# Kernel tuning notes

Measured on AMD Instinct MI355X. Metric: run time of the kernel, lower is better.

The kernel has to match this reference:

```python
import jax, jax.numpy as jnp
import numpy as np

EPS = 1e-6      # delta in ixaxaar/pytorch-dnc util.py and Memory.reset
CLIP = 20.0     # DNC default controller-output clip
M, Wc, R, H, IN, OUT = 10, 20, 1, 256, 27, 128
NN_IN = IN + R * Wc                 # 47 controller input size
IFACE = R * Wc + 3 * Wc + 5 * R + 3  # 88 interface vector size


def _cosine_weights(mem, keys, strengths):
    # mem (B,M,Wc), keys (B,K,Wc), strengths (B,K) -> softmax over cells of scaled cosine sim
    mem_n = mem / (jnp.linalg.norm(mem, axis=2, keepdims=True) + EPS)
    key_n = keys / (jnp.linalg.norm(keys, axis=2, keepdims=True) + EPS)
    d = jnp.einsum('bkw,bmw->bkm', key_n, mem_n)
    return jax.nn.softmax(d * strengths[:, :, None], axis=2)


def _dnc_classifier(x, W_ih, W_hh, b_ih, b_hh, W_xi, b_xi, W_fc, b_fc):
    B, T, _ = x.shape
    # ixaxaar's dnc.py builds inputs[t] = cat(x_t, last_read) ONCE with the initial
    # (zero) last_read, so read vectors never feed the next-step input.
    pad = jnp.zeros((B, R * Wc), x.dtype)
    eye_mask = 1.0 - jnp.eye(M, dtype=x.dtype)

    def step(state, x_t):
        h, c, mem, link, prec, rw, ww, usage = state
        # ---- LSTM controller (1 hidden layer, torch gate order i,f,g,o) ----
        inp = jnp.concatenate([x_t, pad], axis=1)                 # (B,47)
        gates = inp @ W_ih.T + b_ih + h @ W_hh.T + b_hh           # (B,4H)
        i, f, g, o = jnp.split(gates, 4, axis=1)
        c = jax.nn.sigmoid(f) * c + jax.nn.sigmoid(i) * jnp.tanh(g)
        h = jax.nn.sigmoid(o) * jnp.tanh(c)
        out = jnp.clip(h, -CLIP, CLIP)
        # ---- interface vector ----
        xi = out @ W_xi.T + b_xi                                  # (B,88)
        p = R * Wc
        rk = jnp.tanh(xi[:, :p]).reshape(B, R, Wc)                # read keys
        rs = jax.nn.softplus(xi[:, p:p + R]); p += R              # read strengths
        wk = jnp.tanh(xi[:, p:p + Wc]).reshape(B, 1, Wc); p += Wc # write key
        ws = jax.nn.softplus(xi[:, p:p + 1]); p += 1              # write strength
        ev = jax.nn.sigmoid(xi[:, p:p + Wc]); p += Wc             # erase vector
        wv = jnp.tanh(xi[:, p:p + Wc]); p += Wc                   # write vector
        fg = jax.nn.sigmoid(xi[:, p:p + R]); p += R               # free gates
        ag = jax.nn.sigmoid(xi[:, p:p + 1]); p += 1               # allocation gate
        wg = jax.nn.sigmoid(xi[:, p:p + 1]); p += 1               # write gate
        rm = jax.nn.softmax(xi[:, p:p + 3 * R].reshape(B, R, 3), axis=-1)  # read modes (b,f,c)
        # ---- usage (uses PREVIOUS write/read weights) ----
        usage = usage + (1 - usage) * ww
        usage = usage * jnp.prod(1 - fg[:, :, None] * rw, axis=1)
        # ---- write weighting: content + allocation (sort-based free list) ----
        cw = _cosine_weights(mem, wk, ws)[:, 0]                   # (B,M)
        u2 = EPS + (1 - EPS) * usage
        phi = jnp.argsort(u2, axis=1)
        su = jnp.take_along_axis(u2, phi, axis=1)
        prod_excl = jnp.cumprod(jnp.concatenate([jnp.ones((B, 1), u2.dtype), su], axis=1), axis=1)[:, :-1]
        alloc = jnp.take_along_axis((1 - su) * prod_excl, jnp.argsort(phi, axis=1), axis=1)
        ww = wg * (ag * alloc + (1 - ag) * cw)                    # (B,M)
        # ---- erase + write memory ----
        mem = mem * (1 - ww[:, :, None] * ev[:, None, :]) + ww[:, :, None] * wv[:, None, :]
        # ---- temporal link matrix + precedence ----
        link = (1 - ww[:, :, None] - ww[:, None, :]) * link + ww[:, :, None] * prec[:, None, :]
        link = link * eye_mask
        prec = (1 - jnp.sum(ww, axis=1, keepdims=True)) * prec + ww
        # ---- read weighting (content + forward/backward temporal) ----
        cwr = _cosine_weights(mem, rk, rs)                        # (B,R,M)
        fw = jnp.einsum('brm,bnm->brn', rw, link)                 # forward  = L @ w
        bw = jnp.einsum('brm,bmn->brn', rw, link)                 # backward = L^T @ w
        rw = rm[:, :, 0:1] * bw + rm[:, :, 1:2] * fw + rm[:, :, 2:3] * cwr
        return (h, c, mem, link, prec, rw, ww, usage), None

    z = jnp.zeros
    state0 = (z((B, H), x.dtype), z((B, H), x.dtype),
              jnp.full((B, M, Wc), EPS, x.dtype), z((B, M, M), x.dtype),
              z((B, M), x.dtype), jnp.full((B, R, M), EPS, x.dtype),
              jnp.full((B, M), EPS, x.dtype), z((B, M), x.dtype))
    (h, *_), _ = jax.lax.scan(step, state0, jnp.swapaxes(x, 0, 1))
    # classifier head: fc1 on final controller hidden state
    return h @ W_fc.T + b_fc


def setup_inputs() -> dict:
    key = jax.random.key(0)
    ks = jax.random.split(key, 10)
    B, T = 128, 512
    kb = 1.0 / np.sqrt(H)
    u = lambda kk, shape: jax.random.uniform(kk, shape, jnp.float32, -kb, kb)
    return {
        'x': jax.random.normal(ks[0], (B, T, IN), jnp.float32),
        'input_lengths': jax.random.randint(ks[1], (B,), 1, T + 1).astype(jnp.int32),
        'W_ih': u(ks[2], (4 * H, NN_IN)),
        'W_hh': u(ks[3], (4 * H, H)),
        'b_ih': u(ks[4], (4 * H,)),
        'b_hh': u(ks[5], (4 * H,)),
        'W_xi': u(ks[6], (IFACE, H)),
        'b_xi': u(ks[7], (IFACE,)),
        'W_fc': u(ks[8], (OUT, H)),
        'b_fc': u(ks[9], (OUT,)),
    }


def reference(x, input_lengths, W_ih, W_hh, b_ih, b_hh, W_xi, b_xi, W_fc, b_fc):
    # input_lengths is unpacked and discarded by DNCClassifier.forward
    return _dnc_classifier(x, W_ih, W_hh, b_ih, b_hh, W_xi, b_xi, W_fc, b_fc)
```

## Files before the change

### kernel.cpp

```cpp
#include <hip/hip_runtime.h>
#include <hip/hip_fp16.h>


typedef _Float16 h2t __attribute__((ext_vector_type(2)));
typedef unsigned int u32x4 __attribute__((ext_vector_type(4)));

#if defined(__has_builtin)
#  if __has_builtin(__builtin_amdgcn_fdot2)
#    define HAVE_FDOT2 1
#  endif
#endif

__device__ __forceinline__ h2t bc2(unsigned int v) {
  union { unsigned int u; h2t h; } x; x.u = v; return x.h;
}
__device__ __forceinline__ unsigned int pk(float a, float b) {
  union { h2t h; unsigned int u; } x;
  x.h[0] = (_Float16)a; x.h[1] = (_Float16)b;
  return x.u;
}
__device__ __forceinline__ float fdot2f(h2t a, h2t b, float c) {
#ifdef HAVE_FDOT2
  return __builtin_amdgcn_fdot2(a, b, c, false);
#else
  return c + (float)a[0] * (float)b[0] + (float)a[1] * (float)b[1];
#endif
}
__device__ __forceinline__ float dot4(u32x4 w, u32x4 h, float a) {
  a = fdot2f(bc2(w[0]), bc2(h[0]), a);
  a = fdot2f(bc2(w[1]), bc2(h[1]), a);
  a = fdot2f(bc2(w[2]), bc2(h[2]), a);
  a = fdot2f(bc2(w[3]), bc2(h[3]), a);
  return a;
}
__device__ __forceinline__ float sigmf_(float x) {
  return 1.f / (1.f + __expf(-x));
}
__device__ __forceinline__ float tanhf_(float x) {
  float xc = fminf(15.f, fmaxf(-15.f, x));
  float e = __expf(2.f * xc);
  return (e - 1.f) / (e + 1.f);
}

#define WS_P_OFF 0ull
#define WS_W_OFF 134217728ull
#define WS_NEED  134742016ull

__global__ void prep_w(const float* __restrict__ W_hh,
                       unsigned char* __restrict__ ws) {
  int j = blockIdx.x * 256 + threadIdx.x;
  int e = j & 3, v = (j >> 2) & 511, f = j >> 11;
  int jq = f >> 2, g = f & 3;
  int w = v >> 6, l = v & 63;
  int half = w >> 2;
  int u = ((w & 3) << 6) + l;
  int k2 = 64 * half + 4 * jq + e;
  int r = g * 256 + u;
  ((unsigned int*)(ws + WS_W_OFF))[j] =
      pk(W_hh[r * 256 + 2 * k2], W_hh[r * 256 + 2 * k2 + 1]);
}

__global__ __launch_bounds__(256) void prep_p(const float* __restrict__ x,
                                              const float* __restrict__ W_ih,
                                              const float* __restrict__ b_ih,
                                              const float* __restrict__ b_hh,
                                              unsigned char* __restrict__ ws) {
  __shared__ unsigned int sX[64][14];
  const int u = threadIdx.x;
  const int t = blockIdx.x >> 1;
  const int b0 = (blockIdx.x & 1) << 6;
  unsigned int wih[4][14];
  float bias[4];
#pragma unroll
  for (int g = 0; g < 4; ++g) {
    const float* row = W_ih + (size_t)(g * 256 + u) * 47;
    bias[g] = b_ih[g * 256 + u] + b_hh[g * 256 + u];
#pragma unroll
    for (int j = 0; j < 14; ++j) {
      float a = row[2 * j];
      float b = (2 * j + 1 < 27) ? row[2 * j + 1] : 0.f;
      wih[g][j] = pk(a, b);
    }
  }
#pragma unroll 1
  for (int j = u; j < 896; j += 256) {
    int row = j / 14, c2 = j - 14 * row;
    const float* xr = x + ((size_t)(b0 + row) * 512 + t) * 27;
    float a = xr[2 * c2];
    float bb = (2 * c2 + 1 < 27) ? xr[2 * c2 + 1] : 0.f;
    sX[row][c2] = pk(a, bb);
  }
  __syncthreads();
  uint2* Pout = (uint2*)(ws + WS_P_OFF);
#pragma unroll 2
  for (int p = 0; p < 64; ++p) {
    float a0 = bias[0], a1 = bias[1], a2 = bias[2], a3 = bias[3];
#pragma unroll
    for (int j = 0; j < 14; ++j) {
      h2t xx = bc2(sX[p][j]);
      a0 = fdot2f(bc2(wih[0][j]), xx, a0);
      a1 = fdot2f(bc2(wih[1][j]), xx, a1);
      a2 = fdot2f(bc2(wih[2][j]), xx, a2);
      a3 = fdot2f(bc2(wih[3][j]), xx, a3);
    }
    uint2 o; o.x = pk(a0, a1); o.y = pk(a2, a3);
    Pout[((size_t)t * 128 + (b0 + p)) * 256 + u] = o;
  }
}

#define JHB(jq, W0, W1, W2, W3)        \
  {                                    \
    u32x4 hq = rd[jq];                 \
    acc0 = dot4(W0, hq, acc0);         \
    acc1 = dot4(W1, hq, acc1);         \
    acc2 = dot4(W2, hq, acc2);         \
    acc3 = dot4(W3, hq, acc3);         \
  }

__global__ __launch_bounds__(512) void scan_k(
    const unsigned char* __restrict__ ws, const float* __restrict__ W_fc,
    const float* __restrict__ b_fc, float* __restrict__ out) {
  __shared__ u32x4 sW[18 * 512];
  __shared__ u32x4 sHq[2][32];
  __shared__ float4 sRed[256];
  __shared__ float sHF[256];
  const int v = threadIdx.x, b = blockIdx.x;
  const int w = v >> 6, l = v & 63;
  const int half = w >> 2;
  const int u = ((w & 3) << 6) + l;
  const bool upd = (half == 0);
  const u32x4* Wq = (const u32x4*)(ws + WS_W_OFF);

  u32x4 wr[18];
#pragma unroll
  for (int f = 0; f < 18; ++f) wr[f] = Wq[f * 512 + v];
#pragma unroll
  for (int f = 0; f < 18; ++f) sW[f * 512 + v] = Wq[(18 + f) * 512 + v];
  if (v < 64) {
    u32x4 z = {0u, 0u, 0u, 0u};
    ((u32x4*)sHq)[v] = z;
  }

  const uint2* Pbuf = (const uint2*)(ws + WS_P_OFF);
  uint2 pP = make_uint2(0u, 0u);
  if (upd) pP = Pbuf[(size_t)b * 256 + u];
  float c = 0.f, hval = 0.f;
  __syncthreads();

#pragma unroll 1
  for (int t = 0; t < 512; ++t) {
    u32x4 sa0 = Wq[36 * 512 + v], sa1 = Wq[37 * 512 + v];
    u32x4 sa2 = Wq[38 * 512 + v], sa3 = Wq[39 * 512 + v];
    u32x4 sb0 = Wq[40 * 512 + v], sb1 = Wq[41 * 512 + v];
    u32x4 sb2 = Wq[42 * 512 + v], sb3 = Wq[43 * 512 + v];

    const u32x4* rd = &sHq[t & 1][half << 4];
    float acc0 = 0.f, acc1 = 0.f, acc2 = 0.f, acc3 = 0.f;
    JHB(0, wr[0], wr[1], wr[2], wr[3]);
    JHB(1, wr[4], wr[5], wr[6], wr[7]);
    JHB(2, wr[8], wr[9], wr[10], wr[11]);
    JHB(3, wr[12], wr[13], wr[14], wr[15]);
    JHB(4, wr[16], wr[17], sW[0 * 512 + v], sW[1 * 512 + v]);
    JHB(5, sW[2 * 512 + v], sW[3 * 512 + v], sW[4 * 512 + v], sW[5 * 512 + v]);
    JHB(6, sW[6 * 512 + v], sW[7 * 512 + v], sW[8 * 512 + v], sW[9 * 512 + v]);
    JHB(7, sW[10 * 512 + v], sW[11 * 512 + v], sW[12 * 512 + v], sW[13 * 512 + v]);
    JHB(8, sW[14 * 512 + v], sW[15 * 512 + v], sW[16 * 512 + v], sW[17 * 512 + v]);
    JHB(9, sa0, sa1, sa2, sa3);
    sa0 = Wq[44 * 512 + v]; sa1 = Wq[45 * 512 + v];
    sa2 = Wq[46 * 512 + v]; sa3 = Wq[47 * 512 + v];
    JHB(10, sb0, sb1, sb2, sb3);
    sb0 = Wq[48 * 512 + v]; sb1 = Wq[49 * 512 + v];
    sb2 = Wq[50 * 512 + v]; sb3 = Wq[51 * 512 + v];
    JHB(11, sa0, sa1, sa2, sa3);
    sa0 = Wq[52 * 512 + v]; sa1 = Wq[53 * 512 + v];
    sa2 = Wq[54 * 512 + v]; sa3 = Wq[55 * 512 + v];
    JHB(12, sb0, sb1, sb2, sb3);
    sb0 = Wq[56 * 512 + v]; sb1 = Wq[57 * 512 + v];
    sb2 = Wq[58 * 512 + v]; sb3 = Wq[59 * 512 + v];
    JHB(13, sa0, sa1, sa2, sa3);
    sa0 = Wq[60 * 512 + v]; sa1 = Wq[61 * 512 + v];
    sa2 = Wq[62 * 512 + v]; sa3 = Wq[63 * 512 + v];
    JHB(14, sb0, sb1, sb2, sb3);
    JHB(15, sa0, sa1, sa2, sa3);

    if (!upd) sRed[u] = make_float4(acc0, acc1, acc2, acc3);
    __syncthreads();

    if (upd) {
      float4 o = sRed[u];
      h2t p01 = bc2(pP.x), p23 = bc2(pP.y);
      float gi = acc0 + o.x + (float)p01[0];
      float gf = acc1 + o.y + (float)p01[1];
      float gg = acc2 + o.z + (float)p23[0];
      float go = acc3 + o.w + (float)p23[1];
      c = sigmf_(gf) * c + sigmf_(gi) * tanhf_(gg);
      hval = sigmf_(go) * tanhf_(c);
      ((_Float16*)(&sHq[(t + 1) & 1][0]))[u] = (_Float16)hval;
      if (t == 511) sHF[u] = hval;
      int tn = (t < 511) ? t + 1 : 511;
      pP = Pbuf[((size_t)tn * 128 + b) * 256 + u];
    }
    __syncthreads();
  }

  if (v < 128) {
    const float4* wrow = (const float4*)(W_fc + (size_t)v * 256);
    float a = b_fc[v];
#pragma unroll 8
    for (int q = 0; q < 64; ++q) {
      float4 wv = wrow[q];
      float4 hh = ((const float4*)sHF)[q];
      a += wv.x * hh.x + wv.y * hh.y + wv.z * hh.z + wv.w * hh.w;
    }
    out[(size_t)b * 128 + v] = a;
  }
}

extern "C" void kernel_launch(void* const* d_in, const int* in_sizes, int n_in,
                              void* d_out, int out_size, void* d_ws,
                              size_t ws_size, hipStream_t stream) {
  const float* x    = (const float*)d_in[0];
  const float* W_ih = (const float*)d_in[2];
  const float* W_hh = (const float*)d_in[3];
  const float* b_ih = (const float*)d_in[4];
  const float* b_hh = (const float*)d_in[5];
  const float* W_fc = (const float*)d_in[8];
  const float* b_fc = (const float*)d_in[9];
  unsigned char* ws = (unsigned char*)d_ws;

  if (ws_size < WS_NEED) return;

  prep_w<<<512, 256, 0, stream>>>(W_hh, ws);
  prep_p<<<1024, 256, 0, stream>>>(x, W_ih, b_ih, b_hh, ws);
  scan_k<<<128, 512, 0, stream>>>(ws, W_fc, b_fc, (float*)d_out);
}
```

Measured before the change: 913.3 us.

## Process two batch elements per scan block to reuse loaded recurrent weights

Each scan block now handles two batch rows instead of one. Every weight fragment, whether held in registers, LDS or fetched from global memory, is dotted against both hidden states, and each half of the block finishes the gate update for one element. This halves the grid to 64 blocks and doubles the arithmetic per weight load. The cost is more accumulator registers, fewer weights kept in registers (16 instead of 18), and each block's serial per-step critical path roughly doubles in dot-product work.

After: 1.490 ms. 63.2% more time.

```diff
diff --git a/kernel.cpp b/kernel.cpp
--- a/kernel.cpp
+++ b/kernel.cpp
@@ -108,111 +108,115 @@
   }
 }
 
-#define JHB(jq, W0, W1, W2, W3)        \
-  {                                    \
-    u32x4 hq = rd[jq];                 \
-    acc0 = dot4(W0, hq, acc0);         \
-    acc1 = dot4(W1, hq, acc1);         \
-    acc2 = dot4(W2, hq, acc2);         \
-    acc3 = dot4(W3, hq, acc3);         \
+#define JH2(jq, W0, W1, W2, W3)          \
+  {                                      \
+    u32x4 hM = rdM[jq], hO = rdO[jq];    \
+    aM0 = dot4(W0, hM, aM0);             \
+    aO0 = dot4(W0, hO, aO0);             \
+    aM1 = dot4(W1, hM, aM1);             \
+    aO1 = dot4(W1, hO, aO1);             \
+    aM2 = dot4(W2, hM, aM2);             \
+    aO2 = dot4(W2, hO, aO2);             \
+    aM3 = dot4(W3, hM, aM3);             \
+    aO3 = dot4(W3, hO, aO3);             \
   }
 
 __global__ __launch_bounds__(512) void scan_k(
     const unsigned char* __restrict__ ws, const float* __restrict__ W_fc,
     const float* __restrict__ b_fc, float* __restrict__ out) {
   __shared__ u32x4 sW[18 * 512];
-  __shared__ u32x4 sHq[2][32];
-  __shared__ float4 sRed[256];
-  __shared__ float sHF[256];
-  const int v = threadIdx.x, b = blockIdx.x;
+  __shared__ u32x4 sH[2][2][32];
+  __shared__ float4 sRed[2][256];
+  __shared__ float sHF[2][256];
+  const int v = threadIdx.x, b0 = blockIdx.x * 2;
   const int w = v >> 6, l = v & 63;
   const int half = w >> 2;
   const int u = ((w & 3) << 6) + l;
-  const bool upd = (half == 0);
+  const int me = half, ot = half ^ 1;
   const u32x4* Wq = (const u32x4*)(ws + WS_W_OFF);
 
-  u32x4 wr[18];
-#pragma unroll
-  for (int f = 0; f < 18; ++f) wr[f] = Wq[f * 512 + v];
-#pragma unroll
-  for (int f = 0; f < 18; ++f) sW[f * 512 + v] = Wq[(18 + f) * 512 + v];
-  if (v < 64) {
-    u32x4 z = {0u, 0u, 0u, 0u};
-    ((u32x4*)sHq)[v] = z;
-  }
+  u32x4 wr[16];
+#pragma unroll
+  for (int f = 0; f < 16; ++f) wr[f] = Wq[f * 512 + v];
+#pragma unroll
+  for (int f = 0; f < 18; ++f) sW[f * 512 + v] = Wq[(16 + f) * 512 + v];
+  if (v < 128) ((u32x4*)sH)[v] = u32x4{0u, 0u, 0u, 0u};
 
   const uint2* Pbuf = (const uint2*)(ws + WS_P_OFF);
-  uint2 pP = make_uint2(0u, 0u);
-  if (upd) pP = Pbuf[(size_t)b * 256 + u];
+  uint2 pP = Pbuf[((size_t)0 * 128 + (b0 + me)) * 256 + u];
   float c = 0.f, hval = 0.f;
   __syncthreads();
 
 #pragma unroll 1
   for (int t = 0; t < 512; ++t) {
-    u32x4 sa0 = Wq[36 * 512 + v], sa1 = Wq[37 * 512 + v];
-    u32x4 sa2 = Wq[38 * 512 + v], sa3 = Wq[39 * 512 + v];
-    u32x4 sb0 = Wq[40 * 512 + v], sb1 = Wq[41 * 512 + v];
-    u32x4 sb2 = Wq[42 * 512 + v], sb3 = Wq[43 * 512 + v];
-
-    const u32x4* rd = &sHq[t & 1][half << 4];
-    float acc0 = 0.f, acc1 = 0.f, acc2 = 0.f, acc3 = 0.f;
-    JHB(0, wr[0], wr[1], wr[2], wr[3]);
-    JHB(1, wr[4], wr[5], wr[6], wr[7]);
-    JHB(2, wr[8], wr[9], wr[10], wr[11]);
-    JHB(3, wr[12], wr[13], wr[14], wr[15]);
-    JHB(4, wr[16], wr[17], sW[0 * 512 + v], sW[1 * 512 + v]);
-    JHB(5, sW[2 * 512 + v], sW[3 * 512 + v], sW[4 * 512 + v], sW[5 * 512 + v]);
-    JHB(6, sW[6 * 512 + v], sW[7 * 512 + v], sW[8 * 512 + v], sW[9 * 512 + v]);
-    JHB(7, sW[10 * 512 + v], sW[11 * 512 + v], sW[12 * 512 + v], sW[13 * 512 + v]);
-    JHB(8, sW[14 * 512 + v], sW[15 * 512 + v], sW[16 * 512 + v], sW[17 * 512 + v]);
-    JHB(9, sa0, sa1, sa2, sa3);
-    sa0 = Wq[44 * 512 + v]; sa1 = Wq[45 * 512 + v];
-    sa2 = Wq[46 * 512 + v]; sa3 = Wq[47 * 512 + v];
-    JHB(10, sb0, sb1, sb2, sb3);
-    sb0 = Wq[48 * 512 + v]; sb1 = Wq[49 * 512 + v];
-    sb2 = Wq[50 * 512 + v]; sb3 = Wq[51 * 512 + v];
-    JHB(11, sa0, sa1, sa2, sa3);
-    sa0 = Wq[52 * 512 + v]; sa1 = Wq[53 * 512 + v];
-    sa2 = Wq[54 * 512 + v]; sa3 = Wq[55 * 512 + v];
-    JHB(12, sb0, sb1, sb2, sb3);
-    sb0 = Wq[56 * 512 + v]; sb1 = Wq[57 * 512 + v];
-    sb2 = Wq[58 * 512 + v]; sb3 = Wq[59 * 512 + v];
-    JHB(13, sa0, sa1, sa2, sa3);
-    sa0 = Wq[60 * 512 + v]; sa1 = Wq[61 * 512 + v];
-    sa2 = Wq[62 * 512 + v]; sa3 = Wq[63 * 512 + v];
-    JHB(14, sb0, sb1, sb2, sb3);
-    JHB(15, sa0, sa1, sa2, sa3);
-
-    if (!upd) sRed[u] = make_float4(acc0, acc1, acc2, acc3);
+    u32x4 t0 = Wq[34 * 512 + v], t1 = Wq[35 * 512 + v];
+    u32x4 t2 = Wq[36 * 512 + v], t3 = Wq[37 * 512 + v];
+    u32x4 t4 = Wq[38 * 512 + v], t5 = Wq[39 * 512 + v];
+    u32x4 t6 = Wq[40 * 512 + v], t7 = Wq[41 * 512 + v];
+
+    const u32x4* rdM = &sH[me][t & 1][half << 4];
+    const u32x4* rdO = &sH[ot][t & 1][half << 4];
+    float aM0 = 0.f, aM1 = 0.f, aM2 = 0.f, aM3 = 0.f;
+    float aO0 = 0.f, aO1 = 0.f, aO2 = 0.f, aO3 = 0.f;
+    JH2(0, wr[0], wr[1], wr[2], wr[3]);
+    JH2(1, wr[4], wr[5], wr[6], wr[7]);
+    JH2(2, wr[8], wr[9], wr[10], wr[11]);
+    JH2(3, wr[12], wr[13], wr[14], wr[15]);
+    JH2(4, sW[0 * 512 + v], sW[1 * 512 + v], sW[2 * 512 + v], sW[3 * 512 + v]);
+    JH2(5, sW[4 * 512 + v], sW[5 * 512 + v], sW[6 * 512 + v], sW[7 * 512 + v]);
+    JH2(6, sW[8 * 512 + v], sW[9 * 512 + v], sW[10 * 512 + v], sW[11 * 512 + v]);
+    JH2(7, sW[12 * 512 + v], sW[13 * 512 + v], sW[14 * 512 + v], sW[15 * 512 + v]);
+    JH2(8, sW[16 * 512 + v], sW[17 * 512 + v], t0, t1);
+    t0 = Wq[42 * 512 + v]; t1 = Wq[43 * 512 + v];
+    JH2(9, t2, t3, t4, t5);
+    t2 = Wq[44 * 512 + v]; t3 = Wq[45 * 512 + v];
+    t4 = Wq[46 * 512 + v]; t5 = Wq[47 * 512 + v];
+    JH2(10, t6, t7, t0, t1);
+    t6 = Wq[48 * 512 + v]; t7 = Wq[49 * 512 + v];
+    t0 = Wq[50 * 512 + v]; t1 = Wq[51 * 512 + v];
+    JH2(11, t2, t3, t4, t5);
+    t2 = Wq[52 * 512 + v]; t3 = Wq[53 * 512 + v];
+    t4 = Wq[54 * 512 + v]; t5 = Wq[55 * 512 + v];
+    JH2(12, t6, t7, t0, t1);
+    t6 = Wq[56 * 512 + v]; t7 = Wq[57 * 512 + v];
+    t0 = Wq[58 * 512 + v]; t1 = Wq[59 * 512 + v];
+    JH2(13, t2, t3, t4, t5);
+    t2 = Wq[60 * 512 + v]; t3 = Wq[61 * 512 + v];
+    t4 = Wq[62 * 512 + v]; t5 = Wq[63 * 512 + v];
+    JH2(14, t6, t7, t0, t1);
+    JH2(15, t2, t3, t4, t5);
+
+    sRed[ot][u] = make_float4(aO0, aO1, aO2, aO3);
     __syncthreads();
 
-    if (upd) {
-      float4 o = sRed[u];
+    {
+      float4 o = sRed[me][u];
       h2t p01 = bc2(pP.x), p23 = bc2(pP.y);
-      float gi = acc0 + o.x + (float)p01[0];
-      float gf = acc1 + o.y + (float)p01[1];
-      float gg = acc2 + o.z + (float)p23[0];
-      float go = acc3 + o.w + (float)p23[1];
+      float gi = aM0 + o.x + (float)p01[0];
+      float gf = aM1 + o.y + (float)p01[1];
+      float gg = aM2 + o.z + (float)p23[0];
+      float go = aM3 + o.w + (float)p23[1];
       c = sigmf_(gf) * c + sigmf_(gi) * tanhf_(gg);
       hval = sigmf_(go) * tanhf_(c);
-      ((_Float16*)(&sHq[(t + 1) & 1][0]))[u] = (_Float16)hval;
-      if (t == 511) sHF[u] = hval;
+      ((_Float16*)(&sH[me][(t + 1) & 1][0]))[u] = (_Float16)hval;
+      if (t == 511) sHF[me][u] = hval;
       int tn = (t < 511) ? t + 1 : 511;
-      pP = Pbuf[((size_t)tn * 128 + b) * 256 + u];
+      pP = Pbuf[((size_t)tn * 128 + (b0 + me)) * 256 + u];
     }
     __syncthreads();
   }
 
-  if (v < 128) {
-    const float4* wrow = (const float4*)(W_fc + (size_t)v * 256);
-    float a = b_fc[v];
+  if (v < 256) {
+    const int elem = v >> 7, row = v & 127;
+    const float4* wrow = (const float4*)(W_fc + (size_t)row * 256);
+    float a = b_fc[row];
 #pragma unroll 8
     for (int q = 0; q < 64; ++q) {
       float4 wv = wrow[q];
-      float4 hh = ((const float4*)sHF)[q];
+      float4 hh = ((const float4*)&sHF[elem][0])[q];
       a += wv.x * hh.x + wv.y * hh.y + wv.z * hh.z + wv.w * hh.w;
     }
-    out[(size_t)b * 128 + v] = a;
+    out[(size_t)(b0 + elem) * 128 + row] = a;
   }
 }
 
@@ -232,5 +236,5 @@
 
   prep_w<<<512, 256, 0, stream>>>(W_hh, ws);
   prep_p<<<1024, 256, 0, stream>>>(x, W_ih, b_ih, b_hh, ws);
-  scan_k<<<128, 512, 0, stream>>>(ws, W_fc, b_fc, (float*)d_out);
-}
+  scan_k<<<64, 512, 0, stream>>>(ws, W_fc, b_fc, (float*)d_out);
+}
```
